# Performance work log

Hardware: AMD Instinct MI355X
Metric: run time of the kernel (lower is better)

The kernel has to match this reference:

```python
import jax, jax.numpy as jnp
import numpy as np

B, F, E, K, U, D_MODEL, H = 8192, 2048, 16, 2, 2048, 2048, 16
DEPTH = D_MODEL // H


def setup_inputs() -> dict:
    key = jax.random.key(0)
    ks = jax.random.split(key, 12)
    s = 0.02
    return {
        "x": jax.random.normal(ks[0], (B, F), dtype=jnp.float32),
        "router_w": jax.random.normal(ks[1], (F, E), dtype=jnp.float32) * s,
        "router_b": jnp.zeros((E,), dtype=jnp.float32),
        "expert_w": jax.random.normal(ks[2], (E, F, U), dtype=jnp.float32) * s,
        "expert_b": jnp.zeros((E, U), dtype=jnp.float32),
        "wq": jax.random.normal(ks[3], (U, D_MODEL), dtype=jnp.float32) * s,
        "bq": jnp.zeros((D_MODEL,), dtype=jnp.float32),
        "wk": jax.random.normal(ks[4], (U, D_MODEL), dtype=jnp.float32) * s,
        "bk": jnp.zeros((D_MODEL,), dtype=jnp.float32),
        "wv": jax.random.normal(ks[5], (U, D_MODEL), dtype=jnp.float32) * s,
        "bv": jnp.zeros((D_MODEL,), dtype=jnp.float32),
        "wo": jax.random.normal(ks[6], (D_MODEL, D_MODEL), dtype=jnp.float32) * s,
        "bo": jnp.zeros((D_MODEL,), dtype=jnp.float32),
    }


def reference(x, router_w, router_b, expert_w, expert_b,
              wq, bq, wk, bk, wv, bv, wo, bo):
    # ----- MoE block -----
    router_logits = x @ router_w + router_b                 # [B, E]
    router_probs = jax.nn.softmax(router_logits, axis=-1)   # [B, E]
    _, top_k_idx = jax.lax.top_k(router_probs, K)           # [B, K]
    # mask[b, e] = count of e among top-k indices of sample b (0/1 in practice)
    mask = jnp.sum(jax.nn.one_hot(top_k_idx, E, dtype=x.dtype), axis=1)  # [B, E]
    # dense all-expert compute, as in the original module
    expert_out = jax.nn.relu(jnp.einsum('bf,efu->beu', x, expert_w) + expert_b)  # [B, E, U]
    gate = router_probs * mask                               # [B, E]
    moe_out = jnp.einsum('be,beu->bu', gate, expert_out)     # [B, U]

    # ----- MLA block (elementwise attention over a single latent vector) -----
    q = (moe_out @ wq + bq).reshape(B, H, DEPTH)
    k = (moe_out @ wk + bk).reshape(B, H, DEPTH)
    v = (moe_out @ wv + bv).reshape(B, H, DEPTH)
    scores = jnp.sum(q * k, axis=-1, keepdims=True) / jnp.sqrt(jnp.float32(DEPTH))  # [B, H, 1]
    attn = jax.nn.softmax(scores, axis=-2)                   # softmax over heads
    out = (attn * v).reshape(B, H * DEPTH)                   # [B, d_model]
    return out @ wo + bo
```

## Files before the change

### kernel.cpp

```cpp
#include <hip/hip_runtime.h>
#include <hip/hip_bf16.h>
#include <cstdint>

typedef __bf16 bf16;
typedef __bf16 bf16x4 __attribute__((ext_vector_type(4)));
typedef __bf16 bf16x8 __attribute__((ext_vector_type(8)));
typedef float  f32x4  __attribute__((ext_vector_type(4)));

#define BTOK 8192
#define FDIM 2048
#define NEXP 16
#define UDIM 2048
#define DMODEL 2048
#define BSTRIDE 8448

__device__ __forceinline__ void gl2lds16(const void* g, void* l) {
  __builtin_amdgcn_global_load_lds(
      (const __attribute__((address_space(1))) void*)g,
      (__attribute__((address_space(3))) void*)l, 16, 0, 0);
}


#define G256_BAR()  __builtin_amdgcn_s_barrier()
#define G256_LGK0() asm volatile("s_waitcnt lgkmcnt(0)" ::: "memory")

#define G256_STAGE(h, kt) do {                                               \
    const bf16* sb_ = ((h) < 2) ? Ab : Bb;                                   \
    const int ro_ = (((kt) & 1) << 16) + (((h) >= 2) ? 32768 : 0)            \
                    + (((h) & 1) << 13);                                     \
    _Pragma("unroll")                                                        \
    for (int l_ = 0; l_ < 2; ++l_) {                                         \
      const int u_   = (((h) & 1) << 9) + (l_ << 10) + tid;                  \
      const int row_ = (u_ & 1023) >> 2;                                     \
      const int ch_  = ((u_ >> 10) << 2)                                     \
                       + ((u_ & 3) ^ (((row_ >> 3) & 1) << 1));              \
      const bf16* s_ = sb_ + (size_t)(row_ * Kdim + (kt) * 64 + ch_ * 8);    \
      char* d_ = smem + ro_ + (l_ << 14) + ((tid & ~63) << 4);               \
      gl2lds16(s_, d_);                                                      \
    }                                                                        \
  } while (0)

#define E256_STAGE(h, kt) do {                                               \
    const bf16* rp_ = ((h) == 0) ? aRow0 : ((h) == 1) ? aRow1                \
                      : ((h) == 2) ? bRow0 : bRow1;                          \
    const int ro_ = (((kt) & 1) << 16) + (((h) >= 2) ? 32768 : 0)            \
                    + (((h) & 1) << 13);                                     \
    _Pragma("unroll")                                                        \
    for (int l_ = 0; l_ < 2; ++l_) {                                         \
      const bf16* s_ = rp_ + (kt) * 64 + (l_ * 4 + chsw) * 8;                \
      char* d_ = smem + ro_ + (l_ << 14) + ((tid & ~63) << 4);               \
      gl2lds16(s_, d_);                                                      \
    }                                                                        \
  } while (0)

#define G256_LDA(I0)                                                         \
  _Pragma("unroll") for (int i_ = 0; i_ < 4; ++i_)                           \
  _Pragma("unroll") for (int ks_ = 0; ks_ < 2; ++ks_)                        \
    Ar[(I0) + i_][ks_] =                                                     \
        *(const bf16x8*)(smem + c + aOff[(I0) + i_] + ks_ * 16384);

#define G256_LDB(J0)                                                         \
  _Pragma("unroll") for (int jj_ = 0; jj_ < 2; ++jj_)                        \
  _Pragma("unroll") for (int ks_ = 0; ks_ < 2; ++ks_)                        \
    Br[jj_][ks_] =                                                           \
        *(const bf16x8*)(smem + c + bOff[(J0) + jj_] + ks_ * 16384);

#define G256_MFMA16(I0, J0)                                                  \
  _Pragma("unroll") for (int i_ = 0; i_ < 4; ++i_)                           \
  _Pragma("unroll") for (int jj_ = 0; jj_ < 2; ++jj_)                        \
  _Pragma("unroll") for (int ks_ = 0; ks_ < 2; ++ks_)                        \
    acc[(I0) + i_][(J0) + jj_] = __builtin_amdgcn_mfma_f32_16x16x32_bf16(    \
        Ar[(I0) + i_][ks_], Br[jj_][ks_], acc[(I0) + i_][(J0) + jj_], 0, 0, 0);

#define G256_OFFSETS()                                                       \
  int aOff[8], bOff[4];                                                      \
  _Pragma("unroll")                                                          \
  for (int i = 0; i < 8; ++i) {                                              \
    const int row = wm + i * 16 + llo;                                       \
    aOff[i] = (row * 64 + lhi * 16) ^ (((row >> 3) & 1) << 5);               \
  }                                                                          \
  _Pragma("unroll")                                                          \
  for (int j = 0; j < 4; ++j) {                                              \
    const int row = wn + j * 16 + llo;                                       \
    bOff[j] = 32768 + ((row * 64 + lhi * 16) ^ (((row >> 3) & 1) << 5));     \
  }

#define G256_KLOOP(STAGE_M, NT)                                              \
  STAGE_M(0, 0); STAGE_M(1, 0); STAGE_M(2, 0); STAGE_M(3, 0);                \
  STAGE_M(0, 1); STAGE_M(1, 1);                                              \
  asm volatile("s_waitcnt vmcnt(4)" ::: "memory");                           \
  G256_BAR();                                                                \
  _Pragma("unroll 1")                                                        \
  for (int t = 0; t < (NT); ++t) {                                           \
    const int c = (t & 1) << 16;                                             \
    const bool p1 = (t + 1 < (NT)), p2 = (t + 2 < (NT));                     \
    G256_LDA(0); G256_LDB(0);                                                \
    if (p1) STAGE_M(2, t + 1);                                               \
    G256_BAR(); G256_LGK0();                                                 \
    __builtin_amdgcn_s_setprio(1); G256_MFMA16(0, 0); __builtin_amdgcn_s_setprio(0); \
    G256_BAR();                                                              \
    G256_LDA(4);                                                             \
    if (p1) STAGE_M(3, t + 1);                                               \
    G256_BAR(); G256_LGK0();                                                 \
    __builtin_amdgcn_s_setprio(1); G256_MFMA16(4, 0); __builtin_amdgcn_s_setprio(0); \
    G256_BAR();                                                              \
    G256_LDB(2);                                                             \
    if (p2) STAGE_M(0, t + 2);                                               \
    G256_BAR(); G256_LGK0();                                                 \
    __builtin_amdgcn_s_setprio(1); G256_MFMA16(4, 2); __builtin_amdgcn_s_setprio(0); \
    G256_BAR();                                                              \
    if (p2) STAGE_M(1, t + 2);                                               \
    G256_BAR();                                                              \
    __builtin_amdgcn_s_setprio(1); G256_MFMA16(0, 2); __builtin_amdgcn_s_setprio(0); \
    if (p2) { asm volatile("s_waitcnt vmcnt(4)" ::: "memory"); }             \
    else    { asm volatile("s_waitcnt vmcnt(0)" ::: "memory"); }             \
    G256_BAR();                                                              \
  }

template <typename OutT>
__global__ __launch_bounds__(512, 2) void gemm256(
    const bf16* __restrict__ A, const bf16* __restrict__ Bt,
    const float* __restrict__ bias, OutT* __restrict__ C,
    int M, int N, int Kdim)
{
  extern __shared__ __align__(16) char smem[];
  const int tid  = threadIdx.x;
  const int lane = tid & 63;
  const int wave = tid >> 6;
  const int wm   = (wave >> 2) << 7;
  const int wn   = (wave & 3) << 6;
  const int lhi  = lane >> 4, llo = lane & 15;

  const int nbx = N >> 8;
  const int nwg = (M >> 8) * nbx;
  const int q8  = nwg >> 3;
  const int bid = (int)blockIdx.x;
  const int swz = (bid & 7) * q8 + (bid >> 3);
  const int mBase = (swz / nbx) << 8;
  const int nBase = (swz % nbx) << 8;

  const bf16* Ab = A + (size_t)mBase * Kdim;
  const bf16* Bb = Bt + (size_t)nBase * Kdim;
  const int NT = Kdim >> 6;

  G256_OFFSETS();

  f32x4 acc[8][4];
  const f32x4 zero = {0.f, 0.f, 0.f, 0.f};
#pragma unroll
  for (int i = 0; i < 8; ++i)
#pragma unroll
    for (int j = 0; j < 4; ++j) acc[i][j] = zero;

  bf16x8 Ar[8][2], Br[2][2];

  G256_KLOOP(G256_STAGE, NT);

#pragma unroll
  for (int i = 0; i < 8; ++i) {
#pragma unroll
    for (int r = 0; r < 4; ++r) {
      const int row = mBase + wm + i * 16 + lhi * 4 + r;
#pragma unroll
      for (int j = 0; j < 4; ++j) {
        const int col = nBase + wn + j * 16 + llo;
        C[(size_t)row * N + col] = (OutT)(acc[i][j][r] + bias[col]);
      }
    }
  }
}

__global__ __launch_bounds__(512, 2) void expert_gemm256(
    const bf16* __restrict__ xb, const bf16* __restrict__ ewt,
    const float* __restrict__ eb, const int* __restrict__ btok,
    const int2* __restrict__ tmap, const int* __restrict__ ntl3,
    const int* __restrict__ slotBase, int passIdx, int e0glob,
    bf16* __restrict__ eout)
{
  extern __shared__ __align__(16) char smem[];
  const int tstart = ntl3[passIdx], tend = ntl3[passIdx + 1];
  const int t = tstart + (int)blockIdx.y;
  if (t >= tend) return;
  const int2 mp = tmap[t];
  const int e = mp.x, rowStart = mp.y;
  const int nBase = (int)blockIdx.x << 8;
  const int tid  = threadIdx.x;
  const int lane = tid & 63;
  const int wave = tid >> 6;
  const int wm   = (wave >> 2) << 7;
  const int wn   = (wave & 3) << 6;
  const int lhi  = lane >> 4, llo = lane & 15;

  const int r0 = tid >> 2;
  const int bbase = e * BSTRIDE + rowStart;
  const bf16* aRow0 = xb + (size_t)btok[bbase + r0] * FDIM;
  const bf16* aRow1 = xb + (size_t)btok[bbase + 128 + r0] * FDIM;
  const bf16* Bb = ewt + ((size_t)(e - e0glob) << 22);
  const bf16* bRow0 = Bb + (size_t)(nBase + r0) * FDIM;
  const bf16* bRow1 = Bb + (size_t)(nBase + 128 + r0) * FDIM;
  const int chsw = (tid & 3) ^ (((r0 >> 3) & 1) << 1);

  G256_OFFSETS();

  f32x4 acc[8][4];
  const f32x4 zero = {0.f, 0.f, 0.f, 0.f};
#pragma unroll
  for (int i = 0; i < 8; ++i)
#pragma unroll
    for (int j = 0; j < 4; ++j) acc[i][j] = zero;

  bf16x8 Ar[8][2], Br[2][2];

  G256_KLOOP(E256_STAGE, 32);

  const int orow = slotBase[e] + rowStart;
#pragma unroll
  for (int i = 0; i < 8; ++i) {
#pragma unroll
    for (int r = 0; r < 4; ++r) {
      const int row = orow + wm + i * 16 + lhi * 4 + r;
#pragma unroll
      for (int j = 0; j < 4; ++j) {
        const int col = nBase + wn + j * 16 + llo;
        const float v = fmaxf(acc[i][j][r] + eb[e * UDIM + col], 0.f);
        eout[(size_t)row * UDIM + col] = (bf16)v;
      }
    }
  }
}

__global__ __launch_bounds__(256) void moe_combine(
    const bf16* __restrict__ eout, const int* __restrict__ pidx,
    const float* __restrict__ tgate, const int* __restrict__ slotBase,
    bf16* __restrict__ moeb)
{
  const int tok = blockIdx.x;
  const int p0 = pidx[2 * tok], p1 = pidx[2 * tok + 1];
  const int r0 = slotBase[p0 >> 14] + (p0 & 16383);
  const int r1 = slotBase[p1 >> 14] + (p1 & 16383);
  const float g0 = tgate[2 * tok], g1 = tgate[2 * tok + 1];
  const int cb = threadIdx.x * 8;
  bf16x8 a = *(const bf16x8*)(eout + (size_t)r0 * UDIM + cb);
  bf16x8 b = *(const bf16x8*)(eout + (size_t)r1 * UDIM + cb);
  bf16x8 o;
#pragma unroll
  for (int u = 0; u < 8; ++u)
    o[u] = (bf16)(g0 * (float)a[u] + g1 * (float)b[u]);
  *(bf16x8*)(moeb + (size_t)tok * UDIM + cb) = o;
}

__global__ __launch_bounds__(256) void transpose_kernel(
    const float* __restrict__ in, bf16* __restrict__ out,
    int R, int C, long long inZ, long long outZ)
{
  __shared__ float tile[64][65];
  const long long zi = (long long)blockIdx.z * inZ;
  const long long zo = (long long)blockIdx.z * outZ;
  const int r0 = blockIdx.y * 64, c0 = blockIdx.x * 64;
  const int tid = threadIdx.x;
  const int tr = tid >> 4;
  const int tc = (tid & 15) * 4;
#pragma unroll
  for (int it = 0; it < 4; ++it) {
    int r = it * 16 + tr;
    float4 v = *(const float4*)(in + zi + (size_t)(r0 + r) * C + c0 + tc);
    tile[r][tc] = v.x; tile[r][tc + 1] = v.y; tile[r][tc + 2] = v.z; tile[r][tc + 3] = v.w;
  }
  __syncthreads();
#pragma unroll
  for (int it = 0; it < 4; ++it) {
    int c = it * 16 + tr;
    bf16x4 ov;
    ov[0] = (bf16)tile[tc + 0][c];
    ov[1] = (bf16)tile[tc + 1][c];
    ov[2] = (bf16)tile[tc + 2][c];
    ov[3] = (bf16)tile[tc + 3][c];
    *(bf16x4*)(out + zo + (size_t)(c0 + c) * R + r0 + tc) = ov;
  }
}

__global__ __launch_bounds__(256) void concat_bias(
    const float* __restrict__ bq, const float* __restrict__ bk,
    const float* __restrict__ bv, float* __restrict__ out)
{
  int i = blockIdx.x * 256 + threadIdx.x;
  if (i < 2048) out[i] = bq[i];
  else if (i < 4096) out[i] = bk[i - 2048];
  else if (i < 6144) out[i] = bv[i - 4096];
}

__global__ __launch_bounds__(256) void router_kernel(
    const float* __restrict__ x, const float* __restrict__ rw,
    const float* __restrict__ rb, bf16* __restrict__ xb,
    int* __restrict__ cnt, int* __restrict__ btok,
    int* __restrict__ pidx, float* __restrict__ tgate)
{
  const int tid = threadIdx.x, lane = tid & 63, wave = tid >> 6;
  const int tokBase = blockIdx.x * 16 + wave * 4;
  float acc[4][16];
#pragma unroll
  for (int t = 0; t < 4; ++t)
#pragma unroll
    for (int e = 0; e < 16; ++e) acc[t][e] = 0.f;

#pragma unroll 1
  for (int c = 0; c < 8; ++c) {
    const int f = c * 256 + lane * 4;
    float xv[4][4];
#pragma unroll
    for (int t = 0; t < 4; ++t) {
      float4 v = *(const float4*)(x + (size_t)(tokBase + t) * FDIM + f);
      xv[t][0] = v.x; xv[t][1] = v.y; xv[t][2] = v.z; xv[t][3] = v.w;
      bf16x4 b; b[0] = (bf16)v.x; b[1] = (bf16)v.y; b[2] = (bf16)v.z; b[3] = (bf16)v.w;
      *(bf16x4*)(xb + (size_t)(tokBase + t) * FDIM + f) = b;
    }
#pragma unroll
    for (int ff = 0; ff < 4; ++ff) {
      const float* rwr = rw + (size_t)(f + ff) * 16;
      float4 r0 = *(const float4*)(rwr);
      float4 r1 = *(const float4*)(rwr + 4);
      float4 r2 = *(const float4*)(rwr + 8);
      float4 r3 = *(const float4*)(rwr + 12);
      float rr[16] = {r0.x, r0.y, r0.z, r0.w, r1.x, r1.y, r1.z, r1.w,
                      r2.x, r2.y, r2.z, r2.w, r3.x, r3.y, r3.z, r3.w};
#pragma unroll
      for (int t = 0; t < 4; ++t) {
        float xs = xv[t][ff];
#pragma unroll
        for (int e = 0; e < 16; ++e) acc[t][e] = fmaf(xs, rr[e], acc[t][e]);
      }
    }
  }
#pragma unroll
  for (int t = 0; t < 4; ++t)
#pragma unroll
    for (int e = 0; e < 16; ++e) {
      float v = acc[t][e];
      v += __shfl_xor(v, 32); v += __shfl_xor(v, 16); v += __shfl_xor(v, 8);
      v += __shfl_xor(v, 4);  v += __shfl_xor(v, 2);  v += __shfl_xor(v, 1);
      acc[t][e] = v;
    }
  if (lane < 4) {
    const int tok = tokBase + lane;
    float lg[16];
#pragma unroll
    for (int e = 0; e < 16; ++e) lg[e] = acc[lane][e] + rb[e];
    float mx = lg[0];
#pragma unroll
    for (int e = 1; e < 16; ++e) mx = fmaxf(mx, lg[e]);
    float p[16], s = 0.f;
#pragma unroll
    for (int e = 0; e < 16; ++e) { p[e] = __expf(lg[e] - mx); s += p[e]; }
    const float inv = 1.f / s;
    int e0 = 0;
#pragma unroll
    for (int e = 1; e < 16; ++e) if (lg[e] > lg[e0]) e0 = e;
    int e1 = (e0 == 0) ? 1 : 0;
#pragma unroll
    for (int e = 0; e < 16; ++e) { if (e != e0 && lg[e] > lg[e1]) e1 = e; }
    const float g0 = p[e0] * inv, g1 = p[e1] * inv;
    int s0 = atomicAdd(cnt + e0, 1);
    btok[e0 * BSTRIDE + s0] = tok;
    pidx[2 * tok]     = (e0 << 14) | s0;
    tgate[2 * tok]    = g0;
    int s1 = atomicAdd(cnt + e1, 1);
    btok[e1 * BSTRIDE + s1] = tok;
    pidx[2 * tok + 1] = (e1 << 14) | s1;
    tgate[2 * tok + 1] = g1;
  }
}

__global__ void finalize_buckets(const int* __restrict__ cnt, int* __restrict__ btok,
                                 int2* __restrict__ tmap, int* __restrict__ ntl3,
                                 int* __restrict__ slotBase)
{
  __shared__ int tilesS[16];
  const int tid = threadIdx.x;
  if (tid < 16) tilesS[tid] = (cnt[tid] + 255) >> 8;
  __syncthreads();
  for (int e = 0; e < 16; ++e) {
    int c = cnt[e], end = tilesS[e] << 8;
    for (int i = c + tid; i < end; i += 256) btok[e * BSTRIDE + i] = 0;
  }
  if (tid == 0) {
    int s = 0, sA = 0, sb = 0;
    for (int e = 0; e < 16; ++e) {
      slotBase[e] = sb;
      for (int m = 0; m < tilesS[e]; ++m) { tmap[s] = make_int2(e, m << 8); ++s; }
      sb += tilesS[e] << 8;
      if (e == 7) sA = s;
    }
    ntl3[0] = 0; ntl3[1] = sA; ntl3[2] = s;
  }
}

__global__ __launch_bounds__(256) void attn_kernel(
    const bf16* __restrict__ qkv, bf16* __restrict__ aout)
{
  const int lane = threadIdx.x & 63, wave = threadIdx.x >> 6;
  const int tok = blockIdx.x * 4 + wave;
  const bf16* base = qkv + (size_t)tok * (3 * DMODEL);
  const int h = lane >> 2, part = lane & 3;
  const int off = h * 128 + part * 32;
  float dot = 0.f;
#pragma unroll
  for (int c = 0; c < 4; ++c) {
    bf16x8 qv = *(const bf16x8*)(base + off + c * 8);
    bf16x8 kv = *(const bf16x8*)(base + DMODEL + off + c * 8);
#pragma unroll
    for (int u = 0; u < 8; ++u) dot += (float)qv[u] * (float)kv[u];
  }
  dot += __shfl_xor(dot, 1);
  dot += __shfl_xor(dot, 2);
  const float score = dot * 0.08838834764831845f;
  float sc[16];
#pragma unroll
  for (int e = 0; e < 16; ++e) sc[e] = __shfl(score, e * 4);
  float mx = sc[0];
#pragma unroll
  for (int e = 1; e < 16; ++e) mx = fmaxf(mx, sc[e]);
  float sum = 0.f, mex = 0.f;
#pragma unroll
  for (int e = 0; e < 16; ++e) {
    float ex = __expf(sc[e] - mx);
    sum += ex;
    mex = (e == h) ? ex : mex;
  }
  const float attn = mex / sum;
  bf16* op = aout + (size_t)tok * DMODEL + off;
#pragma unroll
  for (int c = 0; c < 4; ++c) {
    bf16x8 vv = *(const bf16x8*)(base + 2 * DMODEL + off + c * 8);
    bf16x8 ov;
#pragma unroll
    for (int u = 0; u < 8; ++u) ov[u] = (bf16)(attn * (float)vv[u]);
    *(bf16x8*)(op + c * 8) = ov;
  }
}

extern "C" void kernel_launch(void* const* d_in, const int* in_sizes, int n_in,
                              void* d_out, int out_size, void* d_ws, size_t ws_size,
                              hipStream_t stream) {
  const float* x   = (const float*)d_in[0];
  const float* rw  = (const float*)d_in[1];
  const float* rb  = (const float*)d_in[2];
  const float* ew  = (const float*)d_in[3];
  const float* eb  = (const float*)d_in[4];
  const float* wq  = (const float*)d_in[5];
  const float* bq  = (const float*)d_in[6];
  const float* wk  = (const float*)d_in[7];
  const float* bk  = (const float*)d_in[8];
  const float* wv  = (const float*)d_in[9];
  const float* bv  = (const float*)d_in[10];
  const float* wo_ = (const float*)d_in[11];
  const float* bo  = (const float*)d_in[12];
  float* out = (float*)d_out;

  static bool attrSet = false;
  if (!attrSet) {
    hipFuncSetAttribute((const void*)gemm256<bf16>,
                        hipFuncAttributeMaxDynamicSharedMemorySize, 131072);
    hipFuncSetAttribute((const void*)gemm256<float>,
                        hipFuncAttributeMaxDynamicSharedMemorySize, 131072);
    hipFuncSetAttribute((const void*)expert_gemm256,
                        hipFuncAttributeMaxDynamicSharedMemorySize, 131072);
    attrSet = true;
  }

  uint8_t* ws = (uint8_t*)d_ws;
  bf16*  ewt   = (bf16*)(ws);
  bf16*  moeb  = (bf16*)(ws);
  bf16*  aout  = (bf16*)(ws);
  bf16*  eout  = (bf16*)(ws + 67108864);
  bf16*  qkv   = (bf16*)(ws + 67108864);
  bf16*  xb    = (bf16*)(ws + 167772160);
  bf16*  qkvt  = (bf16*)(ws + 167772160);
  bf16*  wot   = (bf16*)(ws + 167772160 + 25165824);
  uint8_t* misc = ws + 201326592;
  float* bqkv  = (float*)(misc);            misc += 24576;
  int*   cnt   = (int*)(misc);              misc += 256;
  int*   ntl3  = (int*)(misc);              misc += 256;
  int*   slotBase = (int*)(misc);           misc += 256;
  int2*  tmap  = (int2*)(misc);             misc += 2048;
  int*   btok  = (int*)(misc);              misc += 540672;
  int*   pidx  = (int*)(misc);              misc += 65536;
  float* tgate = (float*)(misc);            misc += 65536;

  hipMemsetAsync(cnt, 0, 64, stream);

  transpose_kernel<<<dim3(32, 32, 8), 256, 0, stream>>>(ew, ewt, FDIM, UDIM, 4194304LL, 4194304LL);
  router_kernel<<<512, 256, 0, stream>>>(x, rw, rb, xb, cnt, btok, pidx, tgate);
  finalize_buckets<<<1, 256, 0, stream>>>(cnt, btok, tmap, ntl3, slotBase);
  expert_gemm256<<<dim3(8, 72), 512, 131072, stream>>>(xb, ewt, eb, btok, tmap, ntl3, slotBase, 0, 0, eout);
  transpose_kernel<<<dim3(32, 32, 8), 256, 0, stream>>>(ew + (size_t)8 * 4194304, ewt, FDIM, UDIM, 4194304LL, 4194304LL);
  expert_gemm256<<<dim3(8, 72), 512, 131072, stream>>>(xb, ewt, eb, btok, tmap, ntl3, slotBase, 1, 8, eout);

  moe_combine<<<8192, 256, 0, stream>>>(eout, pidx, tgate, slotBase, moeb);

  transpose_kernel<<<dim3(32, 32, 1), 256, 0, stream>>>(wq, qkvt,            UDIM, DMODEL, 0, 0);
  transpose_kernel<<<dim3(32, 32, 1), 256, 0, stream>>>(wk, qkvt + 4194304,  UDIM, DMODEL, 0, 0);
  transpose_kernel<<<dim3(32, 32, 1), 256, 0, stream>>>(wv, qkvt + 8388608,  UDIM, DMODEL, 0, 0);
  transpose_kernel<<<dim3(32, 32, 1), 256, 0, stream>>>(wo_, wot, DMODEL, DMODEL, 0, 0);
  concat_bias<<<24, 256, 0, stream>>>(bq, bk, bv, bqkv);

  gemm256<bf16><<<dim3(768), 512, 131072, stream>>>(moeb, qkvt, bqkv, qkv, BTOK, 3 * DMODEL, UDIM);
  attn_kernel<<<2048, 256, 0, stream>>>(qkv, aout);
  gemm256<float><<<dim3(256), 512, 131072, stream>>>(aout, wot, bo, out, BTOK, DMODEL, 2048);
}
```

Measured before the change: 1.121 ms.

## Run all experts in a single GEMM pass when workspace allows

When the workspace is large enough, all 16 expert weight matrices are transposed at once and the expert GEMM runs as one launch over every tile, instead of two half-sized passes. This fills the GPU with more concurrent blocks and removes a serialized transpose-then-GEMM stage, at the cost of a larger workspace layout. If the workspace is too small, a three-pass fallback is used. That fallback adds launches and leaves each grid sparsely populated.

```diff
diff --git a/kernel.cpp b/kernel.cpp
--- a/kernel.cpp
+++ b/kernel.cpp
@@ -173,12 +173,12 @@
 __global__ __launch_bounds__(512, 2) void expert_gemm256(
     const bf16* __restrict__ xb, const bf16* __restrict__ ewt,
     const float* __restrict__ eb, const int* __restrict__ btok,
-    const int2* __restrict__ tmap, const int* __restrict__ ntl3,
-    const int* __restrict__ slotBase, int passIdx, int e0glob,
+    const int2* __restrict__ tmap, const int* __restrict__ ntl,
+    const int* __restrict__ slotBase, int pa, int pb, int e0glob,
     bf16* __restrict__ eout)
 {
   extern __shared__ __align__(16) char smem[];
-  const int tstart = ntl3[passIdx], tend = ntl3[passIdx + 1];
+  const int tstart = ntl[pa], tend = ntl[pb];
   const int t = tstart + (int)blockIdx.y;
   if (t >= tend) return;
   const int2 mp = tmap[t];
@@ -371,7 +371,7 @@
 }
 
 __global__ void finalize_buckets(const int* __restrict__ cnt, int* __restrict__ btok,
-                                 int2* __restrict__ tmap, int* __restrict__ ntl3,
+                                 int2* __restrict__ tmap, int* __restrict__ ntl,
                                  int* __restrict__ slotBase)
 {
   __shared__ int tilesS[16];
@@ -383,14 +383,15 @@
     for (int i = c + tid; i < end; i += 256) btok[e * BSTRIDE + i] = 0;
   }
   if (tid == 0) {
-    int s = 0, sA = 0, sb = 0;
+    int s = 0, s5 = 0, s10 = 0, sb = 0;
     for (int e = 0; e < 16; ++e) {
       slotBase[e] = sb;
       for (int m = 0; m < tilesS[e]; ++m) { tmap[s] = make_int2(e, m << 8); ++s; }
       sb += tilesS[e] << 8;
-      if (e == 7) sA = s;
+      if (e == 5) s5 = s;
+      if (e == 10) s10 = s;
     }
-    ntl3[0] = 0; ntl3[1] = sA; ntl3[2] = s;
+    ntl[0] = 0; ntl[1] = s5; ntl[2] = s10; ntl[3] = s;
   }
 }
 
@@ -468,18 +469,34 @@
   }
 
   uint8_t* ws = (uint8_t*)d_ws;
-  bf16*  ewt   = (bf16*)(ws);
-  bf16*  moeb  = (bf16*)(ws);
-  bf16*  aout  = (bf16*)(ws);
-  bf16*  eout  = (bf16*)(ws + 67108864);
-  bf16*  qkv   = (bf16*)(ws + 67108864);
-  bf16*  xb    = (bf16*)(ws + 167772160);
-  bf16*  qkvt  = (bf16*)(ws + 167772160);
-  bf16*  wot   = (bf16*)(ws + 167772160 + 25165824);
-  uint8_t* misc = ws + 201326592;
+  const bool sp = (ws_size >= 253000000ULL);
+
+  bf16 *ewt, *xb, *eout, *moeb, *qkvt, *wot, *qkv, *aout;
+  uint8_t* misc;
+  if (sp) {
+    ewt  = (bf16*)(ws);
+    eout = (bf16*)(ws + 134217728);
+    xb   = (bf16*)(ws + 218103808);
+    misc = ws + 251658240;
+    moeb = (bf16*)(ws);
+    qkvt = (bf16*)(ws + 33554432);
+    wot  = (bf16*)(ws + 58720256);
+    aout = (bf16*)(ws + 67108864);
+    qkv  = (bf16*)(ws + 134217728);
+  } else {
+    ewt  = (bf16*)(ws);
+    moeb = (bf16*)(ws);
+    aout = (bf16*)(ws);
+    eout = (bf16*)(ws + 67108864);
+    qkv  = (bf16*)(ws + 67108864);
+    xb   = (bf16*)(ws + 167772160);
+    qkvt = (bf16*)(ws + 167772160);
+    wot  = (bf16*)(ws + 167772160 + 25165824);
+    misc = ws + 201326592;
+  }
   float* bqkv  = (float*)(misc);            misc += 24576;
   int*   cnt   = (int*)(misc);              misc += 256;
-  int*   ntl3  = (int*)(misc);              misc += 256;
+  int*   ntl   = (int*)(misc);              misc += 256;
   int*   slotBase = (int*)(misc);           misc += 256;
   int2*  tmap  = (int2*)(misc);             misc += 2048;
   int*   btok  = (int*)(misc);              misc += 540672;
@@ -488,12 +505,24 @@
 
   hipMemsetAsync(cnt, 0, 64, stream);
 
-  transpose_kernel<<<dim3(32, 32, 8), 256, 0, stream>>>(ew, ewt, FDIM, UDIM, 4194304LL, 4194304LL);
   router_kernel<<<512, 256, 0, stream>>>(x, rw, rb, xb, cnt, btok, pidx, tgate);
-  finalize_buckets<<<1, 256, 0, stream>>>(cnt, btok, tmap, ntl3, slotBase);
-  expert_gemm256<<<dim3(8, 72), 512, 131072, stream>>>(xb, ewt, eb, btok, tmap, ntl3, slotBase, 0, 0, eout);
-  transpose_kernel<<<dim3(32, 32, 8), 256, 0, stream>>>(ew + (size_t)8 * 4194304, ewt, FDIM, UDIM, 4194304LL, 4194304LL);
-  expert_gemm256<<<dim3(8, 72), 512, 131072, stream>>>(xb, ewt, eb, btok, tmap, ntl3, slotBase, 1, 8, eout);
+  finalize_buckets<<<1, 256, 0, stream>>>(cnt, btok, tmap, ntl, slotBase);
+
+  if (sp) {
+    transpose_kernel<<<dim3(32, 32, 16), 256, 0, stream>>>(ew, ewt, FDIM, UDIM, 4194304LL, 4194304LL);
+    expert_gemm256<<<dim3(8, 80), 512, 131072, stream>>>(
+        xb, ewt, eb, btok, tmap, ntl, slotBase, 0, 3, 0, eout);
+  } else {
+    transpose_kernel<<<dim3(32, 32, 6), 256, 0, stream>>>(ew, ewt, FDIM, UDIM, 4194304LL, 4194304LL);
+    expert_gemm256<<<dim3(8, 72), 512, 131072, stream>>>(
+        xb, ewt, eb, btok, tmap, ntl, slotBase, 0, 1, 0, eout);
+    transpose_kernel<<<dim3(32, 32, 5), 256, 0, stream>>>(ew + (size_t)6 * 4194304, ewt, FDIM, UDIM, 4194304LL, 4194304LL);
+    expert_gemm256<<<dim3(8, 72), 512, 131072, stream>>>(
+        xb, ewt, eb, btok, tmap, ntl, slotBase, 1, 2, 6, eout);
+    transpose_kernel<<<dim3(32, 32, 5), 256, 0, stream>>>(ew + (size_t)11 * 4194304, ewt, FDIM, UDIM, 4194304LL, 4194304LL);
+    expert_gemm256<<<dim3(8, 72), 512, 131072, stream>>>(
+        xb, ewt, eb, btok, tmap, ntl, slotBase, 2, 3, 11, eout);
+  }
 
   moe_combine<<<8192, 256, 0, stream>>>(eout, pidx, tgate, slotBase, moeb);
 
```

Measured after the change: 1.069 ms. 4.6% less time.
